# Kernel tuning notes

Measured on AMD Instinct MI355X. Metric: run time of the kernel, lower is better.

## Reference

```python
import jax, jax.numpy as jnp
import numpy as np

N1 = 4096
N2 = 4096


def _encoder(x, w1, b1, w2, b2, w3, b3):
    # fc1 -> fc2 -> fc3 -> relu (relu only after fc3, matching the torch code)
    h = x @ w1.T + b1
    h = h @ w2.T + b2
    h = h @ w3.T + b3
    return jax.nn.relu(h)


def _self_attention(x, adj, alpha, W):
    # tmp_i = sum_j [adj_ij==1] * alpha_ij * W * x_j ; tmp_i /= deg_i ; tmp_i += x_i (only if deg_i != 0)
    a = (adj == 1).astype(x.dtype)          # [N, N]
    deg = a.sum(axis=1)                     # [N]
    agg = (a * alpha) @ x                   # [N, 64] masked weighted aggregation
    agg = agg * W[0, 0]
    safe_deg = jnp.maximum(deg, 1.0)
    out = agg / safe_deg[:, None] + x       # residual
    return jnp.where((deg != 0.0)[:, None], out, jnp.zeros_like(out))


def setup_inputs() -> dict:
    key = jax.random.key(0)
    ks = jax.random.split(key, 20)
    s = 0.02  # weight scale to keep activations sane through the 4096->256->128->64 MLP
    inp = {
        "x1": jax.random.normal(ks[0], (N1, N1), jnp.float32),
        "x2": jax.random.normal(ks[1], (N2, N2), jnp.float32),
        "adj1": jax.random.randint(ks[2], (N1, N1), 0, 2, jnp.int32),
        "adj2": jax.random.randint(ks[3], (N2, N2), 0, 2, jnp.int32),
        "e1_w1": jax.random.normal(ks[4], (256, N1), jnp.float32) * s,
        "e1_b1": jnp.zeros((256,), jnp.float32),
        "e1_w2": jax.random.normal(ks[5], (128, 256), jnp.float32) * s,
        "e1_b2": jnp.zeros((128,), jnp.float32),
        "e1_w3": jax.random.normal(ks[6], (64, 128), jnp.float32) * s,
        "e1_b3": jnp.zeros((64,), jnp.float32),
        "e2_w1": jax.random.normal(ks[7], (256, N2), jnp.float32) * s,
        "e2_b1": jnp.zeros((256,), jnp.float32),
        "e2_w2": jax.random.normal(ks[8], (128, 256), jnp.float32) * s,
        "e2_b2": jnp.zeros((128,), jnp.float32),
        "e2_w3": jax.random.normal(ks[9], (64, 128), jnp.float32) * s,
        "e2_b3": jnp.zeros((64,), jnp.float32),
        "W": jax.random.normal(ks[10], (1, 1), jnp.float32),
        "alpha1": jax.random.normal(ks[11], (N1, N1), jnp.float32),
        "clf_w": jax.random.normal(ks[12], (2, (N1 + N2) * 64), jnp.float32) * s,
        "clf_b": jnp.zeros((2,), jnp.float32),
    }
    return inp


def reference(x1, x2, adj1, adj2,
              e1_w1, e1_b1, e1_w2, e1_b2, e1_w3, e1_b3,
              e2_w1, e2_b1, e2_w2, e2_b2, e2_w3, e2_b3,
              W, alpha1, clf_w, clf_b):
    h1 = _encoder(x1, e1_w1, e1_b1, e1_w2, e1_b2, e1_w3, e1_b3)  # [N1, 64]
    h2 = _encoder(x2, e2_w1, e2_b1, e2_w2, e2_b2, e2_w3, e2_b3)  # [N2, 64]
    # NOTE: original torch code uses self.alpha1 for BOTH graphs (alpha2 is unused)
    new1 = _self_attention(h1, adj1, alpha1, W)
    new2 = _self_attention(h2, adj2, alpha1[:N2, :N2], W)
    feat = jnp.concatenate([new1, new2], axis=0).reshape(1, -1)  # [1, (N1+N2)*64]
    return feat @ clf_w.T + clf_b  # [1, 2]
```

## Files before the change

kernel.cpp:

```cpp
#include <hip/hip_runtime.h>
#include <hip/hip_bf16.h>
#include <stdint.h>

#define N 4096

typedef __attribute__((ext_vector_type(4))) float f32x4;
typedef __attribute__((ext_vector_type(8))) short s16x8;

__device__ inline unsigned short f2bf(float f) {
    unsigned int u = __float_as_uint(f);
    u += 0x7fffu + ((u >> 16) & 1u);
    return (unsigned short)(u >> 16);
}
__device__ inline float bf2f(unsigned short h) {
    return __uint_as_float(((unsigned int)h) << 16);
}

__global__ void k0a(const float* __restrict__ w2a, const float* __restrict__ w3a,
                    const float* __restrict__ b1a, const float* __restrict__ b2a, const float* __restrict__ b3a,
                    const float* __restrict__ w2b, const float* __restrict__ w3b,
                    const float* __restrict__ b1b, const float* __restrict__ b2b, const float* __restrict__ b3b,
                    float* __restrict__ T, float* __restrict__ beff) {
    const int g  = blockIdx.x >> 5;
    const int nb = blockIdx.x & 31;
    const float* w2 = g ? w2b : w2a;
    const float* w3 = g ? w3b : w3a;
    const int c  = threadIdx.x;
    const int n0 = nb * 2;
    float a0 = 0.f, a1 = 0.f;
#pragma unroll 8
    for (int r = 0; r < 128; ++r) {
        float w = w2[r * 256 + c];
        a0 += w3[n0 * 128 + r] * w;
        a1 += w3[n0 * 128 + 128 + r] * w;
    }
    float* Tg = T + g * 64 * 256;
    Tg[n0 * 256 + c]       = a0;
    Tg[(n0 + 1) * 256 + c] = a1;

    if (nb == 0) {
        __shared__ float ps[256];
        __shared__ float u[128];
        const float* b1 = g ? b1b : b1a;
        const float* b2 = g ? b2b : b2a;
        const float* b3 = g ? b3b : b3a;
        {
            const int r = threadIdx.x >> 1, half = threadIdx.x & 1;
            float s = 0.f;
#pragma unroll 8
            for (int cc = 0; cc < 128; ++cc) s += w2[r * 256 + half * 128 + cc] * b1[half * 128 + cc];
            ps[threadIdx.x] = s;
        }
        __syncthreads();
        if (threadIdx.x < 128)
            u[threadIdx.x] = ps[2 * threadIdx.x] + ps[2 * threadIdx.x + 1] + b2[threadIdx.x];
        __syncthreads();
        {
            const int n = threadIdx.x >> 2, qr = threadIdx.x & 3;
            float s = 0.f;
#pragma unroll
            for (int r = 0; r < 32; ++r) s += w3[n * 128 + qr * 32 + r] * u[qr * 32 + r];
            ps[threadIdx.x] = s;
        }
        __syncthreads();
        if (threadIdx.x < 64)
            beff[g * 64 + threadIdx.x] = ps[4 * threadIdx.x] + ps[4 * threadIdx.x + 1]
                                       + ps[4 * threadIdx.x + 2] + ps[4 * threadIdx.x + 3] + b3[threadIdx.x];
    }
}

__global__ __launch_bounds__(256) void k0b(const float* __restrict__ w1a, const float* __restrict__ w1b,
                                           const float* __restrict__ T,
                                           unsigned short* __restrict__ Wfrag) {
    const int b  = blockIdx.x;
    const int g = b >> 8, n4 = (b >> 4) & 15, kchunk = b & 15;
    const float* w1 = g ? w1b : w1a;
    const int kx = kchunk * 256 + threadIdx.x;
    const float* Tg = T + (size_t)(g * 64 + n4 * 4) * 256;
    float acc[4] = {0.f, 0.f, 0.f, 0.f};
#pragma unroll 8
    for (int r = 0; r < 256; ++r) {
        float w = w1[(size_t)r * N + kx];
#pragma unroll
        for (int j = 0; j < 4; ++j) acc[j] += Tg[j * 256 + r] * w;
    }
    const int kc = kx >> 6, cc = (kx >> 5) & 1, q = (kx >> 3) & 3, ko = kx & 7;
#pragma unroll
    for (int j = 0; j < 4; ++j) {
        const int n = n4 * 4 + j;
        const int ng = n >> 4, l15 = n & 15;
        const int lane = q * 16 + l15;
        const unsigned short hi = f2bf(acc[j]);
        const unsigned short lo = f2bf(acc[j] - bf2f(hi));
        const size_t unit = ((((size_t)g * 64 + kc) * 4 + ng) * 2 + cc) * 2;
        Wfrag[unit * 512 + lane * 8 + ko]       = hi;
        Wfrag[(unit + 1) * 512 + lane * 8 + ko] = lo;
    }
}

__global__ __launch_bounds__(512, 4) void k1(const float* __restrict__ x1, const float* __restrict__ x2,
                                             const unsigned short* __restrict__ Wfrag,
                                             const float* __restrict__ beff,
                                             float* __restrict__ hf, unsigned short* __restrict__ hfrag) {
    const int b  = blockIdx.x;
    const int g  = b & 1;
    const int i0 = (b >> 1) * 16;
    const float* x = g ? x2 : x1;

    const int t = threadIdx.x;
    const int lane = t & 63, kg = t >> 6;
    const int q = lane >> 4, l15 = lane & 15;

    __shared__ float accs[8][4][64][4];
    __shared__ unsigned short htile[64][16];

    f32x4 acc[4];
#pragma unroll
    for (int ng = 0; ng < 4; ++ng) acc[ng] = (f32x4){0.f, 0.f, 0.f, 0.f};

    const float* xrow = x + (size_t)(i0 + l15) * N;
    for (int kk = 0; kk < 8; ++kk) {
        const int kc = kg * 8 + kk;
#pragma unroll
        for (int c = 0; c < 2; ++c) {
            const int ka = kc * 64 + c * 32 + q * 8;
            float4 a0 = *(const float4*)&xrow[ka];
            float4 a1 = *(const float4*)&xrow[ka + 4];
            s16x8 bh[4], bl[4];
#pragma unroll
            for (int ng = 0; ng < 4; ++ng) {
                const size_t unit = ((((size_t)g * 64 + kc) * 4 + ng) * 2 + c) * 2;
                bh[ng] = *(const s16x8*)&Wfrag[unit * 512 + lane * 8];
                bl[ng] = *(const s16x8*)&Wfrag[(unit + 1) * 512 + lane * 8];
            }
            float xv[8] = {a0.x, a0.y, a0.z, a0.w, a1.x, a1.y, a1.z, a1.w};
            s16x8 ah, al;
#pragma unroll
            for (int j = 0; j < 8; ++j) {
                unsigned short h = f2bf(xv[j]);
                ah[j] = (short)h;
                al[j] = (short)f2bf(xv[j] - bf2f(h));
            }
#pragma unroll
            for (int ng = 0; ng < 4; ++ng) {
                acc[ng] = __builtin_amdgcn_mfma_f32_16x16x32_bf16(al, bh[ng], acc[ng], 0, 0, 0);
                acc[ng] = __builtin_amdgcn_mfma_f32_16x16x32_bf16(ah, bl[ng], acc[ng], 0, 0, 0);
                acc[ng] = __builtin_amdgcn_mfma_f32_16x16x32_bf16(ah, bh[ng], acc[ng], 0, 0, 0);
            }
        }
    }
#pragma unroll
    for (int ng = 0; ng < 4; ++ng)
#pragma unroll
        for (int r = 0; r < 4; ++r) accs[kg][ng][lane][r] = acc[ng][r];
    __syncthreads();

    {
        const int ng = kg & 3, rh = kg >> 2;
        const int n = ng * 16 + l15;
        const float be = beff[g * 64 + n];
#pragma unroll
        for (int rr = 0; rr < 2; ++rr) {
            const int r = rh * 2 + rr;
            float s = 0.f;
#pragma unroll
            for (int k8 = 0; k8 < 8; ++k8) s += accs[k8][ng][lane][r];
            float v = fmaxf(s + be, 0.f);
            const int il = q * 4 + r;
            hf[(size_t)(g * N + i0 + il) * 64 + n] = v;
            htile[n][il] = f2bf(v);
        }
    }
    __syncthreads();

    if (t < 128) {
        const int ng2 = t >> 5, jh = (t >> 4) & 1, l = t & 15;
        uint4 v = *(const uint4*)&htile[ng2 * 16 + l][jh * 8];
        const int jc = i0 >> 6, c = (i0 >> 5) & 1, q0 = (i0 >> 3) & 3;
        const size_t unit = (((size_t)g * 4 + ng2) * 64 + jc) * 2 + c;
        *(uint4*)&hfrag[unit * 512 + (size_t)(q0 + jh) * 128 + l * 8] = v;
    }
}

__global__ __launch_bounds__(512, 2) void k2(const int* __restrict__ adj1, const int* __restrict__ adj2,
                                             const float* __restrict__ alpha, const float* __restrict__ Wp,
                                             const unsigned short* __restrict__ hfrag,
                                             const float* __restrict__ hf,
                                             float* __restrict__ outv) {
    const int i0 = blockIdx.x * 16;
    const int t = threadIdx.x;
    const int lane = t & 63, kg = t >> 6;
    const int q = lane >> 4, l15 = lane & 15;

    __shared__ float accs[8][4][64][4];
    __shared__ float degp[8][64][2];
    __shared__ float degf[2][16];

    f32x4 acc1[4], acc2[4];
#pragma unroll
    for (int ng = 0; ng < 4; ++ng) {
        acc1[ng] = (f32x4){0.f, 0.f, 0.f, 0.f};
        acc2[ng] = (f32x4){0.f, 0.f, 0.f, 0.f};
    }
    int deg1 = 0, deg2 = 0;

    const size_t rowoff = (size_t)(i0 + l15) * N;
    for (int kk = 0; kk < 8; ++kk) {
        const int jc = kg * 8 + kk;
#pragma unroll
        for (int c = 0; c < 2; ++c) {
            const int ka = jc * 64 + c * 32 + q * 8;
            const size_t ao = rowoff + ka;
            float4 a0 = *(const float4*)&alpha[ao];
            float4 a1 = *(const float4*)&alpha[ao + 4];
            int4 j10 = *(const int4*)&adj1[ao];
            int4 j11 = *(const int4*)&adj1[ao + 4];
            int4 j20 = *(const int4*)&adj2[ao];
            int4 j21 = *(const int4*)&adj2[ao + 4];
            s16x8 ha1[4], ha2[4];
#pragma unroll
            for (int ng = 0; ng < 4; ++ng) {
                const size_t u1 = (((size_t)0 * 4 + ng) * 64 + jc) * 2 + c;
                const size_t u2 = (((size_t)1 * 4 + ng) * 64 + jc) * 2 + c;
                ha1[ng] = *(const s16x8*)&hfrag[u1 * 512 + lane * 8];
                ha2[ng] = *(const s16x8*)&hfrag[u2 * 512 + lane * 8];
            }
            float av[8] = {a0.x, a0.y, a0.z, a0.w, a1.x, a1.y, a1.z, a1.w};
            int m1[8] = {j10.x == 1, j10.y == 1, j10.z == 1, j10.w == 1,
                         j11.x == 1, j11.y == 1, j11.z == 1, j11.w == 1};
            int m2[8] = {j20.x == 1, j20.y == 1, j20.z == 1, j20.w == 1,
                         j21.x == 1, j21.y == 1, j21.z == 1, j21.w == 1};
            s16x8 bf1, bf2;
#pragma unroll
            for (int j = 0; j < 8; ++j) {
                short bv = (short)f2bf(av[j]);
                bf1[j] = m1[j] ? bv : (short)0;
                bf2[j] = m2[j] ? bv : (short)0;
                deg1 += m1[j];
                deg2 += m2[j];
            }
#pragma unroll
            for (int ng = 0; ng < 4; ++ng) {
                acc1[ng] = __builtin_amdgcn_mfma_f32_16x16x32_bf16(ha1[ng], bf1, acc1[ng], 0, 0, 0);
                acc2[ng] = __builtin_amdgcn_mfma_f32_16x16x32_bf16(ha2[ng], bf2, acc2[ng], 0, 0, 0);
            }
        }
    }

    degp[kg][lane][0] = (float)deg1;
    degp[kg][lane][1] = (float)deg2;
#pragma unroll
    for (int ng = 0; ng < 4; ++ng)
#pragma unroll
        for (int r = 0; r < 4; ++r) accs[kg][ng][lane][r] = acc1[ng][r];
    __syncthreads();
    if (t < 32) {
        int gg = t >> 4, row = t & 15;
        float s = 0.f;
#pragma unroll
        for (int w = 0; w < 8; ++w)
#pragma unroll
            for (int qq = 0; qq < 4; ++qq) s += degp[w][qq * 16 + row][gg];
        degf[gg][row] = s;
    }
    __syncthreads();

    const float W00 = Wp[0];
    {
        const int ng = kg & 3, rh = kg >> 2;
        const int i = i0 + l15;
        const float dg = degf[0][l15];
#pragma unroll
        for (int rr = 0; rr < 2; ++rr) {
            const int r = rh * 2 + rr;
            float s = 0.f;
#pragma unroll
            for (int k8 = 0; k8 < 8; ++k8) s += accs[k8][ng][lane][r];
            const int n = ng * 16 + q * 4 + r;
            float hv = hf[(size_t)i * 64 + n];
            outv[(size_t)i * 64 + n] = (dg != 0.f) ? (s * W00 / fmaxf(dg, 1.f) + hv) : 0.f;
        }
    }
    __syncthreads();
#pragma unroll
    for (int ng = 0; ng < 4; ++ng)
#pragma unroll
        for (int r = 0; r < 4; ++r) accs[kg][ng][lane][r] = acc2[ng][r];
    __syncthreads();
    {
        const int ng = kg & 3, rh = kg >> 2;
        const int i = i0 + l15;
        const float dg = degf[1][l15];
#pragma unroll
        for (int rr = 0; rr < 2; ++rr) {
            const int r = rh * 2 + rr;
            float s = 0.f;
#pragma unroll
            for (int k8 = 0; k8 < 8; ++k8) s += accs[k8][ng][lane][r];
            const int n = ng * 16 + q * 4 + r;
            float hv = hf[(size_t)(N + i) * 64 + n];
            outv[(size_t)(N + i) * 64 + n] = (dg != 0.f) ? (s * W00 / fmaxf(dg, 1.f) + hv) : 0.f;
        }
    }
}

__global__ __launch_bounds__(256) void k3a(const float* __restrict__ feat, const float* __restrict__ clfw,
                                           float* __restrict__ part) {
    const int t = threadIdx.x;
    const size_t idx = (size_t)blockIdx.x * 2048 + (size_t)t * 8;
    float4 a0 = *(const float4*)&feat[idx];
    float4 a1 = *(const float4*)&feat[idx + 4];
    float4 c0 = *(const float4*)&clfw[idx];
    float4 c1 = *(const float4*)&clfw[idx + 4];
    float4 d0 = *(const float4*)&clfw[524288 + idx];
    float4 d1 = *(const float4*)&clfw[524288 + idx + 4];
    float s0 = a0.x * c0.x + a0.y * c0.y + a0.z * c0.z + a0.w * c0.w
             + a1.x * c1.x + a1.y * c1.y + a1.z * c1.z + a1.w * c1.w;
    float s1 = a0.x * d0.x + a0.y * d0.y + a0.z * d0.z + a0.w * d0.w
             + a1.x * d1.x + a1.y * d1.y + a1.z * d1.z + a1.w * d1.w;
    __shared__ float r0[256], r1[256];
    r0[t] = s0; r1[t] = s1;
    __syncthreads();
    for (int s = 128; s > 0; s >>= 1) {
        if (t < s) { r0[t] += r0[t + s]; r1[t] += r1[t + s]; }
        __syncthreads();
    }
    if (t == 0) { part[blockIdx.x * 2] = r0[0]; part[blockIdx.x * 2 + 1] = r1[0]; }
}

__global__ void k3b(const float* __restrict__ part, const float* __restrict__ clfb,
                    float* __restrict__ outp) {
    const int t = threadIdx.x;
    __shared__ float r0[256], r1[256];
    r0[t] = part[t * 2]; r1[t] = part[t * 2 + 1];
    __syncthreads();
    for (int s = 128; s > 0; s >>= 1) {
        if (t < s) { r0[t] += r0[t + s]; r1[t] += r1[t + s]; }
        __syncthreads();
    }
    if (t == 0) { outp[0] = r0[0] + clfb[0]; outp[1] = r1[0] + clfb[1]; }
}

extern "C" void kernel_launch(void* const* d_in, const int* in_sizes, int n_in,
                              void* d_out, int out_size, void* d_ws, size_t ws_size,
                              hipStream_t stream) {
    const float* x1   = (const float*)d_in[0];
    const float* x2   = (const float*)d_in[1];
    const int*   adj1 = (const int*)d_in[2];
    const int*   adj2 = (const int*)d_in[3];
    const float* e1w1 = (const float*)d_in[4];
    const float* e1b1 = (const float*)d_in[5];
    const float* e1w2 = (const float*)d_in[6];
    const float* e1b2 = (const float*)d_in[7];
    const float* e1w3 = (const float*)d_in[8];
    const float* e1b3 = (const float*)d_in[9];
    const float* e2w1 = (const float*)d_in[10];
    const float* e2b1 = (const float*)d_in[11];
    const float* e2w2 = (const float*)d_in[12];
    const float* e2b2 = (const float*)d_in[13];
    const float* e2w3 = (const float*)d_in[14];
    const float* e2b3 = (const float*)d_in[15];
    const float* Wp   = (const float*)d_in[16];
    const float* alph = (const float*)d_in[17];
    const float* clfw = (const float*)d_in[18];
    const float* clfb = (const float*)d_in[19];

    char* wsb = (char*)d_ws;
    unsigned short* Wfrag = (unsigned short*)(wsb);
    float* newv = (float*)(wsb);
    unsigned short* hfrag = (unsigned short*)(wsb + (2u << 20));
    float* hf   = (float*)(wsb + (3u << 20));
    float* T    = (float*)(wsb + (5u << 20));
    float* beff = (float*)(wsb + (5u << 20) + (1u << 17));
    float* part = (float*)(wsb + (5u << 20) + (1u << 17) + 4096);

    hipLaunchKernelGGL(k0a, dim3(64), dim3(256), 0, stream,
                       e1w2, e1w3, e1b1, e1b2, e1b3, e2w2, e2w3, e2b1, e2b2, e2b3, T, beff);
    hipLaunchKernelGGL(k0b, dim3(512), dim3(256), 0, stream, e1w1, e2w1, T, Wfrag);
    hipLaunchKernelGGL(k1, dim3(512), dim3(512), 0, stream, x1, x2, Wfrag, beff, hf, hfrag);
    hipLaunchKernelGGL(k2, dim3(256), dim3(512), 0, stream, adj1, adj2, alph, Wp, hfrag, hf, newv);
    hipLaunchKernelGGL(k3a, dim3(256), dim3(256), 0, stream, newv, clfw, part);
    hipLaunchKernelGGL(k3b, dim3(1), dim3(256), 0, stream, part, clfb, (float*)d_out);
}
```

Before: 403.3 us.

## Split k2 aggregation over K into four partial blocks with a reduction kernel

The masked-attention aggregation kernel now splits the 4096-long neighbour dimension into four chunks, so it launches 1024 blocks instead of 256. Each block writes partial aggregates and partial degrees to workspace. A new small kernel sums the partials and applies the degree normalisation, W scaling and residual. This aims to fill the GPU's compute units better during the bandwidth-heavy pass over adj and alpha. The cost is extra partial-sum traffic to global memory and one more kernel launch.

```diff
diff --git a/kernel.cpp b/kernel.cpp
--- a/kernel.cpp
+++ b/kernel.cpp
@@ -183,18 +183,18 @@
 }
 
 __global__ __launch_bounds__(512, 2) void k2(const int* __restrict__ adj1, const int* __restrict__ adj2,
-                                             const float* __restrict__ alpha, const float* __restrict__ Wp,
+                                             const float* __restrict__ alpha,
                                              const unsigned short* __restrict__ hfrag,
-                                             const float* __restrict__ hf,
-                                             float* __restrict__ outv) {
-    const int i0 = blockIdx.x * 16;
+                                             float* __restrict__ pagg, float* __restrict__ pdeg) {
+    const int b  = blockIdx.x;
+    const int ks = b & 3;
+    const int i0 = (b >> 2) * 16;
     const int t = threadIdx.x;
     const int lane = t & 63, kg = t >> 6;
     const int q = lane >> 4, l15 = lane & 15;
 
     __shared__ float accs[8][4][64][4];
     __shared__ float degp[8][64][2];
-    __shared__ float degf[2][16];
 
     f32x4 acc1[4], acc2[4];
 #pragma unroll
@@ -205,8 +205,8 @@
     int deg1 = 0, deg2 = 0;
 
     const size_t rowoff = (size_t)(i0 + l15) * N;
-    for (int kk = 0; kk < 8; ++kk) {
-        const int jc = kg * 8 + kk;
+    for (int kk = 0; kk < 2; ++kk) {
+        const int jc = ks * 16 + kg * 2 + kk;
 #pragma unroll
         for (int c = 0; c < 2; ++c) {
             const int ka = jc * 64 + c * 32 + q * 8;
@@ -261,15 +261,12 @@
         for (int w = 0; w < 8; ++w)
 #pragma unroll
             for (int qq = 0; qq < 4; ++qq) s += degp[w][qq * 16 + row][gg];
-        degf[gg][row] = s;
-    }
-    __syncthreads();
-
-    const float W00 = Wp[0];
+        pdeg[(size_t)(gg * 4 + ks) * 4096 + i0 + row] = s;
+    }
+
     {
         const int ng = kg & 3, rh = kg >> 2;
         const int i = i0 + l15;
-        const float dg = degf[0][l15];
 #pragma unroll
         for (int rr = 0; rr < 2; ++rr) {
             const int r = rh * 2 + rr;
@@ -277,8 +274,7 @@
 #pragma unroll
             for (int k8 = 0; k8 < 8; ++k8) s += accs[k8][ng][lane][r];
             const int n = ng * 16 + q * 4 + r;
-            float hv = hf[(size_t)i * 64 + n];
-            outv[(size_t)i * 64 + n] = (dg != 0.f) ? (s * W00 / fmaxf(dg, 1.f) + hv) : 0.f;
+            pagg[(((size_t)ks * 4096 + i) << 6) + n] = s;
         }
     }
     __syncthreads();
@@ -290,7 +286,6 @@
     {
         const int ng = kg & 3, rh = kg >> 2;
         const int i = i0 + l15;
-        const float dg = degf[1][l15];
 #pragma unroll
         for (int rr = 0; rr < 2; ++rr) {
             const int r = rh * 2 + rr;
@@ -298,10 +293,37 @@
 #pragma unroll
             for (int k8 = 0; k8 < 8; ++k8) s += accs[k8][ng][lane][r];
             const int n = ng * 16 + q * 4 + r;
-            float hv = hf[(size_t)(N + i) * 64 + n];
-            outv[(size_t)(N + i) * 64 + n] = (dg != 0.f) ? (s * W00 / fmaxf(dg, 1.f) + hv) : 0.f;
-        }
-    }
+            pagg[(((size_t)(4 + ks) * 4096 + i) << 6) + n] = s;
+        }
+    }
+}
+
+__global__ __launch_bounds__(256) void k2b(const float* __restrict__ pagg, const float* __restrict__ pdeg,
+                                           const float* __restrict__ hf, const float* __restrict__ Wp,
+                                           float* __restrict__ outv) {
+    const int idx = blockIdx.x * 256 + threadIdx.x;
+    const int gi  = idx >> 4;
+    const int nq  = idx & 15;
+    const int g   = gi >> 12, i = gi & 4095;
+    const float W00 = Wp[0];
+
+    float dg = 0.f;
+#pragma unroll
+    for (int ks = 0; ks < 4; ++ks) dg += pdeg[(size_t)(g * 4 + ks) * 4096 + i];
+
+    f32x4 s = (f32x4){0.f, 0.f, 0.f, 0.f};
+#pragma unroll
+    for (int ks = 0; ks < 4; ++ks) {
+        const f32x4 p = *(const f32x4*)&pagg[(((size_t)(g * 4 + ks) * 4096 + i) << 6) + nq * 4];
+        s += p;
+    }
+    const f32x4 hv = *(const f32x4*)&hf[((size_t)gi << 6) + nq * 4];
+    const float dmax = fmaxf(dg, 1.f);
+    f32x4 o;
+#pragma unroll
+    for (int j = 0; j < 4; ++j)
+        o[j] = (dg != 0.f) ? (s[j] * W00 / dmax + hv[j]) : 0.f;
+    *(f32x4*)&outv[((size_t)gi << 6) + nq * 4] = o;
 }
 
 __global__ __launch_bounds__(256) void k3a(const float* __restrict__ feat, const float* __restrict__ clfw,
@@ -373,12 +395,15 @@
     float* T    = (float*)(wsb + (5u << 20));
     float* beff = (float*)(wsb + (5u << 20) + (1u << 17));
     float* part = (float*)(wsb + (5u << 20) + (1u << 17) + 4096);
+    float* pagg = (float*)(wsb + (6u << 20));
+    float* pdeg = (float*)(wsb + (14u << 20));
 
     hipLaunchKernelGGL(k0a, dim3(64), dim3(256), 0, stream,
                        e1w2, e1w3, e1b1, e1b2, e1b3, e2w2, e2w3, e2b1, e2b2, e2b3, T, beff);
     hipLaunchKernelGGL(k0b, dim3(512), dim3(256), 0, stream, e1w1, e2w1, T, Wfrag);
     hipLaunchKernelGGL(k1, dim3(512), dim3(512), 0, stream, x1, x2, Wfrag, beff, hf, hfrag);
-    hipLaunchKernelGGL(k2, dim3(256), dim3(512), 0, stream, adj1, adj2, alph, Wp, hfrag, hf, newv);
+    hipLaunchKernelGGL(k2, dim3(1024), dim3(512), 0, stream, adj1, adj2, alph, hfrag, pagg, pdeg);
+    hipLaunchKernelGGL(k2b, dim3(512), dim3(256), 0, stream, pagg, pdeg, hf, Wp, newv);
     hipLaunchKernelGGL(k3a, dim3(256), dim3(256), 0, stream, newv, clfw, part);
     hipLaunchKernelGGL(k3b, dim3(1), dim3(256), 0, stream, part, clfb, (float*)d_out);
 }
```

Measured after the change: 400.9 us. No clear change (-0.6%).
